# Kernel tuning notes

Hardware: AMD Instinct MI355X
Metric: run time of the kernel (lower is better)

The kernel has to match this reference:

```python
import jax, jax.numpy as jnp
import numpy as np

NEG_BIG = -9e15  # matches torch's -9000000000000000.0 mask value


def setup_inputs() -> dict:
    key = jax.random.key(0)
    k1, k2, k3, k4 = jax.random.split(key, 4)
    B, N, Din, Dout = 4, 4096, 256, 128
    x = jax.random.normal(k1, (B, N, Din), dtype=jnp.float32)
    adj = jax.random.randint(k2, (B, N, N), 0, 2, dtype=jnp.int32)
    weight = jax.random.normal(k3, (Din, Dout), dtype=jnp.float32) * (1.414 * (6.0 / (Din + Dout)) ** 0.5)
    a = jax.random.normal(k4, (2 * Dout, 1), dtype=jnp.float32) * 0.1
    bias = jnp.zeros((Dout,), dtype=jnp.float32)
    return {"x": x, "adj": adj, "weight": weight, "a": a, "bias": bias}


def reference(x, adj, weight, a, bias):
    Dout = weight.shape[1]
    h = jnp.matmul(x, weight)                       # [B, N, Dout]
    Wh1 = jnp.matmul(h, a[:Dout, :])                # [B, N, 1]
    Wh2 = jnp.matmul(h, a[Dout:, :])                # [B, N, 1]
    e = jax.nn.gelu(Wh1 + jnp.swapaxes(Wh2, 1, 2), approximate=False)  # [B, N, N]
    attention = jnp.where(adj > 0, e, NEG_BIG)
    attention = jax.nn.softmax(attention, axis=1)   # softmax over dim=1, as in torch code
    out = jnp.matmul(attention, h)                  # [B, N, Dout]
    out = jax.nn.gelu(out, approximate=False)
    # F.normalize(p=2, dim=1): L2-normalize over the node dimension
    norm = jnp.sqrt(jnp.sum(out * out, axis=1, keepdims=True))
    out = out / jnp.maximum(norm, 1e-12)
    return out + bias
```

## Files before the change

### kernel.cpp

```cpp
#include <hip/hip_runtime.h>
#include <hip/hip_bf16.h>
#include <stdint.h>


#define NN   4096
#define BB   4
#define DIN  256
#define DOUT 128

typedef unsigned short u16;
typedef _Float16 f16x8 __attribute__((ext_vector_type(8)));
typedef __attribute__((ext_vector_type(4))) float f32x4;

__device__ __forceinline__ u16 f2h_bits(float f) {
  _Float16 h = (_Float16)f;
  union { _Float16 h; u16 u; } v; v.h = h;
  return v.u;
}

__device__ __forceinline__ float erf_f(float x) {
  float ax = __builtin_fabsf(x);
  float t  = __builtin_amdgcn_rcpf(__builtin_fmaf(0.3275911f, ax, 1.0f));
  float p  = __builtin_fmaf(1.061405429f, t, -1.453152027f);
  p = __builtin_fmaf(p, t, 1.421413741f);
  p = __builtin_fmaf(p, t, -0.284496736f);
  p = __builtin_fmaf(p, t, 0.254829592f);
  p = p * t;
  float e  = __expf(-ax * ax);
  float er = __builtin_fmaf(-p, e, 1.0f);
  return copysignf(er, x);
}

__device__ __forceinline__ float gelu_f(float z) {
  float hz = 0.5f * z;
  return __builtin_fmaf(hz, erf_f(z * 0.70710678118654752f), hz);
}

__device__ __forceinline__ float exp_gelu(float z) { return __expf(gelu_f(z)); }

__global__ __launch_bounds__(256, 2) void k1_proj(
    const float* __restrict__ x, const float* __restrict__ weight,
    const float* __restrict__ a, u16* __restrict__ hT,
    float* __restrict__ Wh1, float* __restrict__ Wh2)
{
  __shared__ float xs[32 * 256];
  __shared__ float T[128 * 33];
  __shared__ float P2a[8 * 32], P2b[8 * 32];

  const int b = blockIdx.y, n0 = blockIdx.x * 32;
  const int tid = threadIdx.x;

  const float4* xsrc = (const float4*)(x + ((size_t)b * NN + n0) * DIN);
  float4* xd = (float4*)xs;
#pragma unroll
  for (int v = 0; v < 8; ++v) xd[tid + v * 256] = xsrc[tid + v * 256];
  __syncthreads();

  const int dg = tid & 31, rg = tid >> 5;
  float acc[4][4] = {};
  const float4* W4 = (const float4*)weight;
#pragma unroll 4
  for (int k = 0; k < 256; ++k) {
    float4 wr = W4[k * 32 + dg];
#pragma unroll
    for (int rr = 0; rr < 4; ++rr) {
      float xv = xs[(rg * 4 + rr) * 256 + k];
      acc[rr][0] = fmaf(xv, wr.x, acc[rr][0]);
      acc[rr][1] = fmaf(xv, wr.y, acc[rr][1]);
      acc[rr][2] = fmaf(xv, wr.z, acc[rr][2]);
      acc[rr][3] = fmaf(xv, wr.w, acc[rr][3]);
    }
  }
#pragma unroll
  for (int rr = 0; rr < 4; ++rr)
#pragma unroll
    for (int dd = 0; dd < 4; ++dd)
      T[(dg * 4 + dd) * 33 + rg * 4 + rr] = acc[rr][dd];
  __syncthreads();

  {
    const int d = tid & 127, half = tid >> 7;
    unsigned int uu[8];
#pragma unroll
    for (int p = 0; p < 8; ++p) {
      float f0 = T[d * 33 + half * 16 + p * 2];
      float f1 = T[d * 33 + half * 16 + p * 2 + 1];
      uu[p] = (unsigned int)f2h_bits(f0) | ((unsigned int)f2h_bits(f1) << 16);
    }
    u16* dst = hT + ((size_t)b * DOUT + d) * NN + n0 + half * 16;
    ((uint4*)dst)[0] = make_uint4(uu[0], uu[1], uu[2], uu[3]);
    ((uint4*)dst)[1] = make_uint4(uu[4], uu[5], uu[6], uu[7]);
  }
  {
    const int r = tid & 31, g8 = tid >> 5;
    float p1 = 0.f, p2 = 0.f;
#pragma unroll
    for (int q = 0; q < 16; ++q) {
      int d = g8 * 16 + q;
      float hv = T[d * 33 + r];
      p1 = fmaf(hv, a[d], p1);
      p2 = fmaf(hv, a[DOUT + d], p2);
    }
    P2a[g8 * 32 + r] = p1;
    P2b[g8 * 32 + r] = p2;
  }
  __syncthreads();
  if (tid < 32) {
    float s1 = 0.f, s2 = 0.f;
#pragma unroll
    for (int g8 = 0; g8 < 8; ++g8) { s1 += P2a[g8 * 32 + tid]; s2 += P2b[g8 * 32 + tid]; }
    Wh1[b * NN + n0 + tid] = s1;
    Wh2[b * NN + n0 + tid] = s2;
  }
}

__global__ __launch_bounds__(256, 2) void k2_fused(
    const int* __restrict__ adj, const float* __restrict__ Wh1,
    const float* __restrict__ Wh2, float* __restrict__ S,
    unsigned int* __restrict__ m32)
{
  const int b = blockIdx.z, jt = blockIdx.x, ic = blockIdx.y;
  const int tid = threadIdx.x;
  const int j = jt * 256 + tid;
  const int lane = tid & 63;
  const int jg = jt * 4 + (tid >> 6);
  const int i0 = ic * 512;

  const float wh2 = Wh2[b * NN + j];
  const int* ap = adj + ((size_t)b * NN + i0) * NN + j;
  const float* w1p = Wh1 + b * NN + i0;
  unsigned int* mlo = m32 + ((size_t)b * 128 + jg * 2) * NN + i0;
  unsigned int* mhi = mlo + NN;

  float s = 0.f;
  for (int g = 0; g < 8; ++g) {
    unsigned long long acc64 = 0ull;
#pragma unroll
    for (int gg = 0; gg < 8; ++gg) {
      int av[8]; float w1v[8];
#pragma unroll
      for (int k = 0; k < 8; ++k) {
        const int ii = g * 64 + gg * 8 + k;
        av[k]  = ap[(size_t)ii * NN];
        w1v[k] = w1p[ii];
      }
#pragma unroll
      for (int k = 0; k < 8; ++k) {
        const unsigned long long bal = __ballot(av[k] > 0);
        if (lane == gg * 8 + k) acc64 = bal;
        const float E = exp_gelu(w1v[k] + wh2);
        s += (av[k] > 0) ? E : 0.f;
      }
    }
    mlo[g * 64 + lane] = (unsigned int)acc64;
    mhi[g * 64 + lane] = (unsigned int)(acc64 >> 32);
  }
  atomicAdd(&S[b * NN + j], s);
}

__global__ __launch_bounds__(256) void k25_rcp(const float* __restrict__ S,
                                               float* __restrict__ Sinv)
{
  int id = blockIdx.x * 256 + threadIdx.x;
  Sinv[id] = 1.0f / S[id];
}

__global__ __launch_bounds__(256, 2) void k3_attn(
    const unsigned int* __restrict__ m32, const float* __restrict__ Wh1,
    const float* __restrict__ Wh2, const float* __restrict__ Sinv,
    const u16* __restrict__ hT, float* __restrict__ out_pre)
{
  __shared__ __align__(16) u16 buf[4][128 * 32];

  const int b = blockIdx.y;
  const int i0 = blockIdx.x * 32;
  const int tid = threadIdx.x;
  const int w = tid >> 6, lane = tid & 63;
  const int m = lane & 15, quad = lane >> 4;

  const float w1a = Wh1[b * NN + i0 + m];
  const float w1b = Wh1[b * NN + i0 + 16 + m];
  const unsigned int* mbase = m32 + (size_t)b * 128 * NN;
  const u16* hTb = hT + (size_t)b * DOUT * NN;
  const u16* srcbase = hTb + (size_t)(lane >> 2) * NN + (lane & 3) * 8;

  f32x4 acc0[8], acc1[8];
#pragma unroll
  for (int t = 0; t < 8; ++t) {
    acc0[t] = (f32x4){0.f, 0.f, 0.f, 0.f};
    acc1[t] = (f32x4){0.f, 0.f, 0.f, 0.f};
  }

  for (int c = 0; c < 32; ++c) {
    const int j0 = w * 1024 + c * 32;
    const int jw = j0 >> 5;

    __builtin_amdgcn_s_waitcnt(0xC07F);
#pragma unroll
    for (int inst = 0; inst < 8; ++inst) {
      const u16* g = srcbase + (size_t)inst * 16 * NN + j0;
      __builtin_amdgcn_global_load_lds(
          (const __attribute__((address_space(1))) void*)g,
          (__attribute__((address_space(3))) void*)&buf[w][inst * 512],
          16, 0, 0);
    }

    const unsigned int Ma = mbase[(size_t)jw * NN + i0 + m];
    const unsigned int Mb = mbase[(size_t)jw * NN + i0 + 16 + m];
    const unsigned int mba = (Ma >> (quad * 8)) & 0xFFu;
    const unsigned int mbb = (Mb >> (quad * 8)) & 0xFFu;

    const int jq = j0 + quad * 8;
    const float4* wp = (const float4*)(Wh2 + b * NN + jq);
    float4 w2a = wp[0], w2b = wp[1];
    const float4* sp = (const float4*)(Sinv + b * NN + jq);
    float4 sva = sp[0], svb = sp[1];

    float q[8];
    f16x8 ah_a, al_a, ah_b, al_b;

    q[0] = (mba & 1u)   ? exp_gelu(w1a + w2a.x) * sva.x : 0.f;
    q[1] = (mba & 2u)   ? exp_gelu(w1a + w2a.y) * sva.y : 0.f;
    q[2] = (mba & 4u)   ? exp_gelu(w1a + w2a.z) * sva.z : 0.f;
    q[3] = (mba & 8u)   ? exp_gelu(w1a + w2a.w) * sva.w : 0.f;
    q[4] = (mba & 16u)  ? exp_gelu(w1a + w2b.x) * svb.x : 0.f;
    q[5] = (mba & 32u)  ? exp_gelu(w1a + w2b.y) * svb.y : 0.f;
    q[6] = (mba & 64u)  ? exp_gelu(w1a + w2b.z) * svb.z : 0.f;
    q[7] = (mba & 128u) ? exp_gelu(w1a + w2b.w) * svb.w : 0.f;
#pragma unroll
    for (int e = 0; e < 8; ++e) {
      _Float16 hi = (_Float16)q[e];
      ah_a[e] = hi;
      al_a[e] = (_Float16)(q[e] - (float)hi);
    }
    q[0] = (mbb & 1u)   ? exp_gelu(w1b + w2a.x) * sva.x : 0.f;
    q[1] = (mbb & 2u)   ? exp_gelu(w1b + w2a.y) * sva.y : 0.f;
    q[2] = (mbb & 4u)   ? exp_gelu(w1b + w2a.z) * sva.z : 0.f;
    q[3] = (mbb & 8u)   ? exp_gelu(w1b + w2a.w) * sva.w : 0.f;
    q[4] = (mbb & 16u)  ? exp_gelu(w1b + w2b.x) * svb.x : 0.f;
    q[5] = (mbb & 32u)  ? exp_gelu(w1b + w2b.y) * svb.y : 0.f;
    q[6] = (mbb & 64u)  ? exp_gelu(w1b + w2b.z) * svb.z : 0.f;
    q[7] = (mbb & 128u) ? exp_gelu(w1b + w2b.w) * svb.w : 0.f;
#pragma unroll
    for (int e = 0; e < 8; ++e) {
      _Float16 hi = (_Float16)q[e];
      ah_b[e] = hi;
      al_b[e] = (_Float16)(q[e] - (float)hi);
    }

    __builtin_amdgcn_s_waitcnt(0x0F70);

#pragma unroll
    for (int t = 0; t < 8; ++t) {
      f16x8 bf = *(const f16x8*)&buf[w][(t * 16 + m) * 32 + quad * 8];
      acc0[t] = __builtin_amdgcn_mfma_f32_16x16x32_f16(ah_a, bf, acc0[t], 0, 0, 0);
      acc0[t] = __builtin_amdgcn_mfma_f32_16x16x32_f16(al_a, bf, acc0[t], 0, 0, 0);
      acc1[t] = __builtin_amdgcn_mfma_f32_16x16x32_f16(ah_b, bf, acc1[t], 0, 0, 0);
      acc1[t] = __builtin_amdgcn_mfma_f32_16x16x32_f16(al_b, bf, acc1[t], 0, 0, 0);
    }
  }

  float* red = (float*)&buf[0][0];
#pragma unroll
  for (int rt = 0; rt < 2; ++rt) {
    __syncthreads();
#pragma unroll
    for (int t = 0; t < 8; ++t)
#pragma unroll
      for (int r = 0; r < 4; ++r)
        red[w * 2048 + (t * 4 + r) * 64 + lane] = rt ? acc1[t][r] : acc0[t][r];
    __syncthreads();
#pragma unroll
    for (int tt = 0; tt < 2; ++tt) {
      const int t = w * 2 + tt;
#pragma unroll
      for (int r = 0; r < 4; ++r) {
        const int o = (t * 4 + r) * 64 + lane;
        float v = red[o] + red[2048 + o] + red[4096 + o] + red[6144 + o];
        out_pre[((size_t)b * NN + i0 + rt * 16 + quad * 4 + r) * DOUT + t * 16 + m] = v;
      }
    }
  }
}

__global__ __launch_bounds__(256) void k4a_gelu_norm(
    const float* __restrict__ out_pre, float* __restrict__ gout,
    float* __restrict__ norm2)
{
  __shared__ float pbuf[256];
  const int b = blockIdx.y;
  const int i0 = blockIdx.x * 64;
  const int tid = threadIdx.x;
  const int d = tid & 127, rh = tid >> 7;
  float acc = 0.f;
  for (int ii = rh; ii < 64; ii += 2) {
    size_t idx = ((size_t)b * NN + i0 + ii) * DOUT + d;
    float g = gelu_f(out_pre[idx]);
    gout[idx] = g;
    acc = fmaf(g, g, acc);
  }
  pbuf[tid] = acc;
  __syncthreads();
  if (tid < 128) atomicAdd(&norm2[b * DOUT + tid], pbuf[tid] + pbuf[tid + 128]);
}

__global__ __launch_bounds__(256) void k4b_scale(
    float* __restrict__ out, const float* __restrict__ norm2,
    const float* __restrict__ bias)
{
  int id = blockIdx.x * 256 + threadIdx.x;
  int d = id & 127;
  int b = id >> 19;
  float nrm = sqrtf(norm2[b * DOUT + d]);
  float sc = 1.0f / fmaxf(nrm, 1e-12f);
  out[id] = fmaf(out[id], sc, bias[d]);
}

extern "C" void kernel_launch(void* const* d_in, const int* in_sizes, int n_in,
                              void* d_out, int out_size, void* d_ws, size_t ws_size,
                              hipStream_t stream)
{
  const float* x      = (const float*)d_in[0];
  const int*   adj    = (const int*)d_in[1];
  const float* weight = (const float*)d_in[2];
  const float* a      = (const float*)d_in[3];
  const float* bias   = (const float*)d_in[4];
  float* out = (float*)d_out;

  char* ws = (char*)d_ws;
  u16*   hT     = (u16*)ws;
  float* Wh1    = (float*)(ws + (size_t)4 * 1024 * 1024);
  float* Wh2    = Wh1 + BB * NN;
  float* S      = Wh2 + BB * NN;
  float* Sinv   = S + BB * NN;
  unsigned int* m32 = (unsigned int*)(Sinv + BB * NN);
  float* out_pre = (float*)((char*)m32 + (size_t)BB * 128 * NN * 4);
  float* norm2   = out_pre + (size_t)BB * NN * DOUT;

  hipMemsetAsync(S, 0, (size_t)BB * NN * sizeof(float), stream);
  hipMemsetAsync(norm2, 0, (size_t)BB * DOUT * sizeof(float), stream);

  k1_proj<<<dim3(NN / 32, BB), 256, 0, stream>>>(x, weight, a, hT, Wh1, Wh2);
  k2_fused<<<dim3(16, 8, BB), 256, 0, stream>>>(adj, Wh1, Wh2, S, m32);
  k25_rcp<<<dim3(BB * NN / 256), 256, 0, stream>>>(S, Sinv);
  k3_attn<<<dim3(NN / 32, BB), 256, 0, stream>>>(m32, Wh1, Wh2, Sinv, hT, out_pre);
  k4a_gelu_norm<<<dim3(64, BB), 256, 0, stream>>>(out_pre, out, norm2);
  k4b_scale<<<dim3((BB * NN * DOUT) / 256), 256, 0, stream>>>(out, norm2, bias);
}
```

Measured before the change: 515.6 us.

## Fuse GELU and norm reduction into attention kernel, drop fp16 split, retile k2

The attention kernel now applies GELU and accumulates per-column squared norms directly, writing final pre-scale output and removing the separate gelu/norm kernel and the out_pre buffer round trip. The hi/lo fp16 split of attention weights is dropped, halving MFMA count but reducing precision of the probabilities to plain fp16. The adjacency scan kernel is retiled to more blocks with fewer rows each and larger load batches, raising parallelism over the dominant adj read.

Result: no change. 506.6 us (-1.8%).

```diff
diff --git a/kernel.cpp b/kernel.cpp
--- a/kernel.cpp
+++ b/kernel.cpp
@@ -114,7 +114,7 @@
   }
 }
 
-__global__ __launch_bounds__(256, 2) void k2_fused(
+__global__ __launch_bounds__(256) void k2_fused(
     const int* __restrict__ adj, const float* __restrict__ Wh1,
     const float* __restrict__ Wh2, float* __restrict__ S,
     unsigned int* __restrict__ m32)
@@ -124,7 +124,7 @@
   const int j = jt * 256 + tid;
   const int lane = tid & 63;
   const int jg = jt * 4 + (tid >> 6);
-  const int i0 = ic * 512;
+  const int i0 = ic * 128;
 
   const float wh2 = Wh2[b * NN + j];
   const int* ap = adj + ((size_t)b * NN + i0) * NN + j;
@@ -133,21 +133,21 @@
   unsigned int* mhi = mlo + NN;
 
   float s = 0.f;
-  for (int g = 0; g < 8; ++g) {
+  for (int g = 0; g < 2; ++g) {
     unsigned long long acc64 = 0ull;
 #pragma unroll
-    for (int gg = 0; gg < 8; ++gg) {
-      int av[8]; float w1v[8];
-#pragma unroll
-      for (int k = 0; k < 8; ++k) {
-        const int ii = g * 64 + gg * 8 + k;
+    for (int gg = 0; gg < 4; ++gg) {
+      int av[16]; float w1v[16];
+#pragma unroll
+      for (int k = 0; k < 16; ++k) {
+        const int ii = g * 64 + gg * 16 + k;
         av[k]  = ap[(size_t)ii * NN];
         w1v[k] = w1p[ii];
       }
 #pragma unroll
-      for (int k = 0; k < 8; ++k) {
+      for (int k = 0; k < 16; ++k) {
         const unsigned long long bal = __ballot(av[k] > 0);
-        if (lane == gg * 8 + k) acc64 = bal;
+        if (lane == gg * 16 + k) acc64 = bal;
         const float E = exp_gelu(w1v[k] + wh2);
         s += (av[k] > 0) ? E : 0.f;
       }
@@ -168,7 +168,8 @@
 __global__ __launch_bounds__(256, 2) void k3_attn(
     const unsigned int* __restrict__ m32, const float* __restrict__ Wh1,
     const float* __restrict__ Wh2, const float* __restrict__ Sinv,
-    const u16* __restrict__ hT, float* __restrict__ out_pre)
+    const u16* __restrict__ hT, float* __restrict__ out,
+    float* __restrict__ norm2)
 {
   __shared__ __align__(16) u16 buf[4][128 * 32];
 
@@ -216,37 +217,23 @@
     const float4* sp = (const float4*)(Sinv + b * NN + jq);
     float4 sva = sp[0], svb = sp[1];
 
-    float q[8];
-    f16x8 ah_a, al_a, ah_b, al_b;
-
-    q[0] = (mba & 1u)   ? exp_gelu(w1a + w2a.x) * sva.x : 0.f;
-    q[1] = (mba & 2u)   ? exp_gelu(w1a + w2a.y) * sva.y : 0.f;
-    q[2] = (mba & 4u)   ? exp_gelu(w1a + w2a.z) * sva.z : 0.f;
-    q[3] = (mba & 8u)   ? exp_gelu(w1a + w2a.w) * sva.w : 0.f;
-    q[4] = (mba & 16u)  ? exp_gelu(w1a + w2b.x) * svb.x : 0.f;
-    q[5] = (mba & 32u)  ? exp_gelu(w1a + w2b.y) * svb.y : 0.f;
-    q[6] = (mba & 64u)  ? exp_gelu(w1a + w2b.z) * svb.z : 0.f;
-    q[7] = (mba & 128u) ? exp_gelu(w1a + w2b.w) * svb.w : 0.f;
-#pragma unroll
-    for (int e = 0; e < 8; ++e) {
-      _Float16 hi = (_Float16)q[e];
-      ah_a[e] = hi;
-      al_a[e] = (_Float16)(q[e] - (float)hi);
-    }
-    q[0] = (mbb & 1u)   ? exp_gelu(w1b + w2a.x) * sva.x : 0.f;
-    q[1] = (mbb & 2u)   ? exp_gelu(w1b + w2a.y) * sva.y : 0.f;
-    q[2] = (mbb & 4u)   ? exp_gelu(w1b + w2a.z) * sva.z : 0.f;
-    q[3] = (mbb & 8u)   ? exp_gelu(w1b + w2a.w) * sva.w : 0.f;
-    q[4] = (mbb & 16u)  ? exp_gelu(w1b + w2b.x) * svb.x : 0.f;
-    q[5] = (mbb & 32u)  ? exp_gelu(w1b + w2b.y) * svb.y : 0.f;
-    q[6] = (mbb & 64u)  ? exp_gelu(w1b + w2b.z) * svb.z : 0.f;
-    q[7] = (mbb & 128u) ? exp_gelu(w1b + w2b.w) * svb.w : 0.f;
-#pragma unroll
-    for (int e = 0; e < 8; ++e) {
-      _Float16 hi = (_Float16)q[e];
-      ah_b[e] = hi;
-      al_b[e] = (_Float16)(q[e] - (float)hi);
-    }
+    f16x8 ah_a, ah_b;
+    ah_a[0] = (_Float16)((mba & 1u)   ? exp_gelu(w1a + w2a.x) * sva.x : 0.f);
+    ah_a[1] = (_Float16)((mba & 2u)   ? exp_gelu(w1a + w2a.y) * sva.y : 0.f);
+    ah_a[2] = (_Float16)((mba & 4u)   ? exp_gelu(w1a + w2a.z) * sva.z : 0.f);
+    ah_a[3] = (_Float16)((mba & 8u)   ? exp_gelu(w1a + w2a.w) * sva.w : 0.f);
+    ah_a[4] = (_Float16)((mba & 16u)  ? exp_gelu(w1a + w2b.x) * svb.x : 0.f);
+    ah_a[5] = (_Float16)((mba & 32u)  ? exp_gelu(w1a + w2b.y) * svb.y : 0.f);
+    ah_a[6] = (_Float16)((mba & 64u)  ? exp_gelu(w1a + w2b.z) * svb.z : 0.f);
+    ah_a[7] = (_Float16)((mba & 128u) ? exp_gelu(w1a + w2b.w) * svb.w : 0.f);
+    ah_b[0] = (_Float16)((mbb & 1u)   ? exp_gelu(w1b + w2a.x) * sva.x : 0.f);
+    ah_b[1] = (_Float16)((mbb & 2u)   ? exp_gelu(w1b + w2a.y) * sva.y : 0.f);
+    ah_b[2] = (_Float16)((mbb & 4u)   ? exp_gelu(w1b + w2a.z) * sva.z : 0.f);
+    ah_b[3] = (_Float16)((mbb & 8u)   ? exp_gelu(w1b + w2a.w) * sva.w : 0.f);
+    ah_b[4] = (_Float16)((mbb & 16u)  ? exp_gelu(w1b + w2b.x) * svb.x : 0.f);
+    ah_b[5] = (_Float16)((mbb & 32u)  ? exp_gelu(w1b + w2b.y) * svb.y : 0.f);
+    ah_b[6] = (_Float16)((mbb & 64u)  ? exp_gelu(w1b + w2b.z) * svb.z : 0.f);
+    ah_b[7] = (_Float16)((mbb & 128u) ? exp_gelu(w1b + w2b.w) * svb.w : 0.f);
 
     __builtin_amdgcn_s_waitcnt(0x0F70);
 
@@ -254,13 +241,12 @@
     for (int t = 0; t < 8; ++t) {
       f16x8 bf = *(const f16x8*)&buf[w][(t * 16 + m) * 32 + quad * 8];
       acc0[t] = __builtin_amdgcn_mfma_f32_16x16x32_f16(ah_a, bf, acc0[t], 0, 0, 0);
-      acc0[t] = __builtin_amdgcn_mfma_f32_16x16x32_f16(al_a, bf, acc0[t], 0, 0, 0);
       acc1[t] = __builtin_amdgcn_mfma_f32_16x16x32_f16(ah_b, bf, acc1[t], 0, 0, 0);
-      acc1[t] = __builtin_amdgcn_mfma_f32_16x16x32_f16(al_b, bf, acc1[t], 0, 0, 0);
     }
   }
 
   float* red = (float*)&buf[0][0];
+  float p2[2] = {0.f, 0.f};
 #pragma unroll
   for (int rt = 0; rt < 2; ++rt) {
     __syncthreads();
@@ -277,31 +263,20 @@
       for (int r = 0; r < 4; ++r) {
         const int o = (t * 4 + r) * 64 + lane;
         float v = red[o] + red[2048 + o] + red[4096 + o] + red[6144 + o];
-        out_pre[((size_t)b * NN + i0 + rt * 16 + quad * 4 + r) * DOUT + t * 16 + m] = v;
+        float gv = gelu_f(v);
+        out[((size_t)b * NN + i0 + rt * 16 + quad * 4 + r) * DOUT + t * 16 + m] = gv;
+        p2[tt] = fmaf(gv, gv, p2[tt]);
       }
     }
   }
-}
-
-__global__ __launch_bounds__(256) void k4a_gelu_norm(
-    const float* __restrict__ out_pre, float* __restrict__ gout,
-    float* __restrict__ norm2)
-{
-  __shared__ float pbuf[256];
-  const int b = blockIdx.y;
-  const int i0 = blockIdx.x * 64;
-  const int tid = threadIdx.x;
-  const int d = tid & 127, rh = tid >> 7;
-  float acc = 0.f;
-  for (int ii = rh; ii < 64; ii += 2) {
-    size_t idx = ((size_t)b * NN + i0 + ii) * DOUT + d;
-    float g = gelu_f(out_pre[idx]);
-    gout[idx] = g;
-    acc = fmaf(g, g, acc);
-  }
-  pbuf[tid] = acc;
-  __syncthreads();
-  if (tid < 128) atomicAdd(&norm2[b * DOUT + tid], pbuf[tid] + pbuf[tid + 128]);
+#pragma unroll
+  for (int tt = 0; tt < 2; ++tt) {
+    float ps = p2[tt];
+    ps += __shfl_xor(ps, 16);
+    ps += __shfl_xor(ps, 32);
+    if (quad == 0)
+      atomicAdd(&norm2[b * DOUT + (w * 2 + tt) * 16 + m], ps);
+  }
 }
 
 __global__ __launch_bounds__(256) void k4b_scale(
@@ -334,16 +309,14 @@
   float* S      = Wh2 + BB * NN;
   float* Sinv   = S + BB * NN;
   unsigned int* m32 = (unsigned int*)(Sinv + BB * NN);
-  float* out_pre = (float*)((char*)m32 + (size_t)BB * 128 * NN * 4);
-  float* norm2   = out_pre + (size_t)BB * NN * DOUT;
+  float* norm2  = (float*)((char*)m32 + (size_t)BB * 128 * NN * 4);
 
   hipMemsetAsync(S, 0, (size_t)BB * NN * sizeof(float), stream);
   hipMemsetAsync(norm2, 0, (size_t)BB * DOUT * sizeof(float), stream);
 
   k1_proj<<<dim3(NN / 32, BB), 256, 0, stream>>>(x, weight, a, hT, Wh1, Wh2);
-  k2_fused<<<dim3(16, 8, BB), 256, 0, stream>>>(adj, Wh1, Wh2, S, m32);
+  k2_fused<<<dim3(16, 32, BB), 256, 0, stream>>>(adj, Wh1, Wh2, S, m32);
   k25_rcp<<<dim3(BB * NN / 256), 256, 0, stream>>>(S, Sinv);
-  k3_attn<<<dim3(NN / 32, BB), 256, 0, stream>>>(m32, Wh1, Wh2, Sinv, hT, out_pre);
-  k4a_gelu_norm<<<dim3(64, BB), 256, 0, stream>>>(out_pre, out, norm2);
+  k3_attn<<<dim3(NN / 32, BB), 256, 0, stream>>>(m32, Wh1, Wh2, Sinv, hT, out, norm2);
   k4b_scale<<<dim3((BB * NN * DOUT) / 256), 256, 0, stream>>>(out, norm2, bias);
 }
```
